# Kernel optimization log

Hardware: AMD Instinct MI355X
Metric: run time of the kernel (lower is better)

Reference implementation:

```python
import jax, jax.numpy as jnp
import numpy as np

N_USER, N_ITEM = 100000, 50000
D, H, B, E = 64, 64, 16384, 2000000

def _xavier(key, shape):
    fan_in, fan_out = shape[0], shape[1]
    lim = float(np.sqrt(6.0 / (fan_in + fan_out)))
    return jax.random.uniform(key, shape, jnp.float32, -lim, lim)

def setup_inputs() -> dict:
    key = jax.random.key(0)
    ks = jax.random.split(key, 16)
    inp = {
        "user_table": _xavier(ks[0], (N_USER, D)),
        "item_table": _xavier(ks[1], (N_ITEM, D)),
        "Wu": _xavier(ks[2], (D, D)),   # GCN_user weight ([in,out])
        "bu": jnp.zeros((D,), jnp.float32),
        "Wi": _xavier(ks[3], (D, D)),   # GCN_item weight
        "bi": jnp.zeros((D,), jnp.float32),
        "W1": _xavier(ks[4], (4 * D, 2 * H)),
        "b1": jnp.zeros((2 * H,), jnp.float32),
        "W2": _xavier(ks[5], (2 * H, H)),
        "b2": jnp.zeros((H,), jnp.float32),
        "W3": _xavier(ks[6], (H, 1)),
        "b3": jnp.zeros((1,), jnp.float32),
        "user_bias": jnp.zeros((N_USER, 1), jnp.float32),
        "item_bias": jnp.zeros((N_ITEM, 1), jnp.float32),
        "user_id": jax.random.randint(ks[7], (B,), 0, N_USER),
        "item_id": jax.random.randint(ks[8], (B,), 0, N_ITEM),
        "edge_user": jax.random.randint(ks[9], (E,), 0, N_USER),
        "edge_item": jax.random.randint(ks[10], (E,), 0, N_ITEM),
    }
    return inp

def reference(user_table, item_table, Wu, bu, Wi, bi, W1, b1, W2, b2, W3, b3,
              user_bias, item_bias, user_id, item_id, edge_user, edge_item):
    # sparse.mm(edge_ui, item_h)[user_id]: aggregate item embeddings per user
    agg_i = jax.ops.segment_sum(item_table[edge_item], edge_user, num_segments=N_USER)[user_id]
    agg_u = jax.ops.segment_sum(user_table[edge_user], edge_item, num_segments=N_ITEM)[item_id]
    ones_e = jnp.ones((edge_user.shape[0],), jnp.float32)
    deg_u = jax.ops.segment_sum(ones_e, edge_user, num_segments=N_USER)[user_id] + 1.0  # item_din
    deg_i = jax.ops.segment_sum(ones_e, edge_item, num_segments=N_ITEM)[item_id] + 1.0  # user_din
    gcn_item_h = agg_i / deg_u[:, None]   # [B, D]
    gcn_user_h = agg_u / deg_i[:, None]   # [B, D]
    # dropout p=0.3 is identity in eval mode
    gcn_user_out = jax.nn.relu(gcn_user_h @ Wu + bu)
    gcn_item_out = jax.nn.relu(gcn_item_h @ Wi + bi)
    u_emb = user_table[user_id]
    i_emb = item_table[item_id]
    x = jnp.concatenate([u_emb * i_emb,
                         u_emb * gcn_item_out,
                         gcn_user_out * i_emb,
                         gcn_user_out * gcn_item_out], axis=-1)  # [B, 4D]
    x1 = jnp.tanh(x @ W1 + b1)
    x2 = jnp.tanh(x1 @ W2 + b2)
    x3 = (x2 @ W3 + b3).reshape(-1)
    return x3 + user_bias[user_id, 0] + item_bias[item_id, 0]
```

## Files before the change

kernel.cpp:

```cpp
#include <hip/hip_runtime.h>
#include <cstdint>
#include <cstddef>

#define D 64
#define CAPU 96
#define CAPI 128
#define OCAP 4096
#define GR 32

__global__ __launch_bounds__(256) void k_build_maps(const int* __restrict__ user_id,
                                                    const int* __restrict__ item_id,
                                                    int* __restrict__ map_u,
                                                    int* __restrict__ map_i, int B)
{
    int i = blockIdx.x * blockDim.x + threadIdx.x;
    if (i < B) {
        atomicCAS(&map_u[user_id[i]], -1, i);
        atomicCAS(&map_i[item_id[i]], -1, i);
    }
}

__global__ __launch_bounds__(256) void k_scatter(const int* __restrict__ edge_user,
                                                 const int* __restrict__ edge_item,
                                                 const int* __restrict__ map_u,
                                                 const int* __restrict__ map_i,
                                                 int* __restrict__ cntU,
                                                 int* __restrict__ cntI,
                                                 uint32_t* __restrict__ listU,
                                                 uint32_t* __restrict__ listI,
                                                 int* __restrict__ ovfCnt,
                                                 uint32_t* __restrict__ ovf, int E)
{
    int t = blockIdx.x * blockDim.x + threadIdx.x;
    int base = t * 4;
    if (base >= E) return;

    int us[4], is[4];
    int cnt4 = 4;
    if (base + 3 < E) {
        int4 eu = *(const int4*)(edge_user + base);
        int4 ei = *(const int4*)(edge_item + base);
        us[0] = eu.x; us[1] = eu.y; us[2] = eu.z; us[3] = eu.w;
        is[0] = ei.x; is[1] = ei.y; is[2] = ei.z; is[3] = ei.w;
    } else {
        cnt4 = E - base;
        for (int q = 0; q < cnt4; ++q) { us[q] = edge_user[base + q]; is[q] = edge_item[base + q]; }
    }

    #pragma unroll
    for (int q = 0; q < 4; ++q) {
        if (q >= cnt4) break;
        int u = us[q], it = is[q];
        int su = map_u[u];
        int si = map_i[it];
        if (su >= 0) {
            int pos = atomicAdd(&cntU[su * 16], 1);
            if (pos < CAPU) listU[(size_t)su * CAPU + pos] = (uint32_t)it;
            else { int o = atomicAdd(ovfCnt, 1);
                   if (o < OCAP) ovf[o] = ((uint32_t)su << 17) | (uint32_t)it; }
        }
        if (si >= 0) {
            int pos = atomicAdd(&cntI[si * 16], 1);
            if (pos < CAPI) listI[(size_t)si * CAPI + pos] = (uint32_t)u;
            else { int o = atomicAdd(ovfCnt, 1);
                   if (o < OCAP) ovf[o] = 0x80000000u | ((uint32_t)si << 17) | (uint32_t)u; }
        }
    }
}

__global__ __launch_bounds__(256) void k_gather(const uint32_t* __restrict__ listU,
                                                const uint32_t* __restrict__ listI,
                                                const int* __restrict__ cntU,
                                                const int* __restrict__ cntI,
                                                const float* __restrict__ user_table,
                                                const float* __restrict__ item_table,
                                                const int* __restrict__ ovfCnt,
                                                const uint32_t* __restrict__ ovf,
                                                float* __restrict__ aggIU,
                                                float* __restrict__ aggUI, int B)
{
    int gg = (blockIdx.x * blockDim.x + threadIdx.x) >> 4;
    if (gg >= 2 * B) return;
    int l16 = threadIdx.x & 15;
    int side = gg >= B;
    int slot = side ? gg - B : gg;

    int cnt = side ? cntI[slot * 16] : cntU[slot * 16];
    int caps = side ? CAPI : CAPU;
    int n = cnt < caps ? cnt : caps;
    const uint32_t* list = side ? (listI + (size_t)slot * CAPI)
                                : (listU + (size_t)slot * CAPU);
    const float4* table4 = (const float4*)(side ? user_table : item_table);

    float4 a0 = {0.f, 0.f, 0.f, 0.f};
    float4 a1 = {0.f, 0.f, 0.f, 0.f};
    int j = 0;
    #pragma unroll 2
    for (; j + 2 <= n; j += 2) {
        int r0 = (int)list[j];
        int r1 = (int)list[j + 1];
        float4 v0 = table4[(size_t)r0 * 16 + l16];
        float4 v1 = table4[(size_t)r1 * 16 + l16];
        a0.x += v0.x; a0.y += v0.y; a0.z += v0.z; a0.w += v0.w;
        a1.x += v1.x; a1.y += v1.y; a1.z += v1.z; a1.w += v1.w;
    }
    if (j < n) {
        int r0 = (int)list[j];
        float4 v0 = table4[(size_t)r0 * 16 + l16];
        a0.x += v0.x; a0.y += v0.y; a0.z += v0.z; a0.w += v0.w;
    }
    if (cnt > caps) {
        int on = *ovfCnt; if (on > OCAP) on = OCAP;
        for (int k = 0; k < on; ++k) {
            uint32_t p = ovf[k];
            if ((int)(p >> 31) == side && (int)((p >> 17) & 0x3FFFu) == slot) {
                float4 v = table4[(size_t)(p & 0x1FFFFu) * 16 + l16];
                a0.x += v.x; a0.y += v.y; a0.z += v.z; a0.w += v.w;
            }
        }
    }
    float inv = 1.0f / ((float)cnt + 1.0f);
    float4 acc = {(a0.x + a1.x) * inv, (a0.y + a1.y) * inv,
                  (a0.z + a1.z) * inv, (a0.w + a1.w) * inv};
    float4* agg4 = (float4*)(side ? aggUI : aggIU);
    agg4[(size_t)slot * 16 + l16] = acc;
}

__global__ __launch_bounds__(256) void k_gcn(const int* __restrict__ user_id,
                                             const int* __restrict__ item_id,
                                             const int* __restrict__ map_u,
                                             const int* __restrict__ map_i,
                                             const float* __restrict__ aggIU,
                                             const float* __restrict__ aggUI,
                                             const float* __restrict__ Wi,
                                             const float* __restrict__ bi,
                                             const float* __restrict__ Wu,
                                             const float* __restrict__ bu,
                                             float* __restrict__ Xgi,
                                             float* __restrict__ Xgu, int B)
{
    __shared__ float A[GR][68];
    __shared__ float Wl[64][64];
    __shared__ int sslot[GR];
    int t = threadIdx.x;
    int nb = B / GR;
    int b = blockIdx.x;
    int side = b >= nb;
    int row0 = (side ? b - nb : b) * GR;

    if (t < GR) {
        int r = row0 + t;
        sslot[t] = side ? map_i[item_id[r]] : map_u[user_id[r]];
    }
    {
        const float4* Wg = (const float4*)(side ? Wu : Wi);
        float4* Wl4 = (float4*)&Wl[0][0];
        #pragma unroll
        for (int q = 0; q < 4; ++q) Wl4[t + q * 256] = Wg[t + q * 256];
    }
    __syncthreads();
    {
        const float4* agg4 = (const float4*)(side ? aggUI : aggIU);
        #pragma unroll
        for (int q = 0; q < 2; ++q) {
            int idx = t * 2 + q;
            int r = idx >> 4, l16 = idx & 15;
            ((float4*)&A[r][0])[l16] = agg4[(size_t)sslot[r] * 16 + l16];
        }
    }
    __syncthreads();

    const float* bias = side ? bu : bi;
    int tx = t & 15, ty = t >> 4;
    float acc[2][4] = {};
    for (int k = 0; k < 64; ++k) {
        float a0 = A[2 * ty][k];
        float a1 = A[2 * ty + 1][k];
        #pragma unroll
        for (int c = 0; c < 4; ++c) {
            float w = Wl[k][tx + 16 * c];
            acc[0][c] = fmaf(a0, w, acc[0][c]);
            acc[1][c] = fmaf(a1, w, acc[1][c]);
        }
    }
    float* Xg = side ? Xgu : Xgi;
    #pragma unroll
    for (int r = 0; r < 2; ++r) {
        int row = row0 + 2 * ty + r;
        #pragma unroll
        for (int c = 0; c < 4; ++c) {
            int col = tx + 16 * c;
            Xg[(size_t)row * 64 + col] = fmaxf(acc[r][c] + bias[col], 0.f);
        }
    }
}

__global__ __launch_bounds__(256) void k_mlp(const int* __restrict__ user_id,
                                             const int* __restrict__ item_id,
                                             const float* __restrict__ user_table,
                                             const float* __restrict__ item_table,
                                             const float* __restrict__ Xgi,
                                             const float* __restrict__ Xgu,
                                             const float* __restrict__ W1,
                                             const float* __restrict__ b1,
                                             const float* __restrict__ W2,
                                             const float* __restrict__ b2,
                                             const float* __restrict__ W3,
                                             const float* __restrict__ b3,
                                             const float* __restrict__ user_bias,
                                             const float* __restrict__ item_bias,
                                             float* __restrict__ out, int B)
{
    __shared__ float Fbuf[64][68];
    __shared__ float WB[8192];
    __shared__ int sU[GR], sI[GR];
    int t = threadIdx.x;
    int row0 = blockIdx.x * GR;
    if (t < GR) { sU[t] = user_id[row0 + t]; sI[t] = item_id[row0 + t]; }
    __syncthreads();

    int tx1 = t & 31, ty1 = t >> 5;
    float acc1[4][4] = {};

    const int fkA[4] = {0, 0, 3, 3};
    const int fkB[4] = {1, 2, 1, 2};
    for (int j = 0; j < 4; ++j) {
        #pragma unroll
        for (int half = 0; half < 2; ++half) {
            int kind = half ? fkB[j] : fkA[j];
            #pragma unroll
            for (int q = 0; q < 2; ++q) {
                int idx = t * 2 + q;
                int r = idx >> 4, l16 = idx & 15;
                const float4* src;
                size_t rowidx;
                if (kind == 0)      { src = (const float4*)user_table; rowidx = (size_t)sU[r]; }
                else if (kind == 1) { src = (const float4*)item_table; rowidx = (size_t)sI[r]; }
                else if (kind == 2) { src = (const float4*)Xgi; rowidx = (size_t)(row0 + r); }
                else                { src = (const float4*)Xgu; rowidx = (size_t)(row0 + r); }
                ((float4*)&Fbuf[half * 32 + r][0])[l16] = src[rowidx * 16 + l16];
            }
        }
        {
            const float4* w4 = (const float4*)W1 + (size_t)j * 2048;
            float4* d = (float4*)WB;
            #pragma unroll
            for (int q = 0; q < 8; ++q) d[t + q * 256] = w4[t + q * 256];
        }
        __syncthreads();
        for (int k = 0; k < 64; ++k) {
            float a[4], b[4];
            #pragma unroll
            for (int r = 0; r < 4; ++r)
                a[r] = Fbuf[4 * ty1 + r][k] * Fbuf[32 + 4 * ty1 + r][k];
            #pragma unroll
            for (int c = 0; c < 4; ++c) b[c] = WB[k * 128 + tx1 + 32 * c];
            #pragma unroll
            for (int r = 0; r < 4; ++r)
                #pragma unroll
                for (int c = 0; c < 4; ++c)
                    acc1[r][c] = fmaf(a[r], b[c], acc1[r][c]);
        }
        __syncthreads();
    }

    float* x1t = &Fbuf[0][0];
    #pragma unroll
    for (int r = 0; r < 4; ++r)
        #pragma unroll
        for (int c = 0; c < 4; ++c) {
            int col = tx1 + 32 * c;
            x1t[(4 * ty1 + r) * 132 + col] = tanhf(acc1[r][c] + b1[col]);
        }
    {
        const float4* w4 = (const float4*)W2;
        float4* d = (float4*)WB;
        #pragma unroll
        for (int q = 0; q < 8; ++q) d[t + q * 256] = w4[t + q * 256];
    }
    __syncthreads();

    int tx2 = t & 15, ty2 = t >> 4;
    float acc2[2][4] = {};
    for (int k = 0; k < 128; ++k) {
        float a0 = x1t[(2 * ty2) * 132 + k];
        float a1 = x1t[(2 * ty2 + 1) * 132 + k];
        #pragma unroll
        for (int c = 0; c < 4; ++c) {
            float w = WB[k * 64 + tx2 + 16 * c];
            acc2[0][c] = fmaf(a0, w, acc2[0][c]);
            acc2[1][c] = fmaf(a1, w, acc2[1][c]);
        }
    }
    float b3v = b3[0];
    #pragma unroll
    for (int r = 0; r < 2; ++r) {
        int lr = 2 * ty2 + r;
        float p = 0.f;
        #pragma unroll
        for (int c = 0; c < 4; ++c) {
            int col = tx2 + 16 * c;
            p += tanhf(acc2[r][c] + b2[col]) * W3[col];
        }
        p += __shfl_xor(p, 1);
        p += __shfl_xor(p, 2);
        p += __shfl_xor(p, 4);
        p += __shfl_xor(p, 8);
        if (tx2 == 0)
            out[row0 + lr] = p + b3v + user_bias[sU[lr]] + item_bias[sI[lr]];
    }
}

extern "C" void kernel_launch(void* const* d_in, const int* in_sizes, int n_in,
                              void* d_out, int out_size, void* d_ws, size_t ws_size,
                              hipStream_t stream)
{
    const float* user_table = (const float*)d_in[0];
    const float* item_table = (const float*)d_in[1];
    const float* Wu = (const float*)d_in[2];
    const float* bu = (const float*)d_in[3];
    const float* Wi = (const float*)d_in[4];
    const float* bi = (const float*)d_in[5];
    const float* W1 = (const float*)d_in[6];
    const float* b1 = (const float*)d_in[7];
    const float* W2 = (const float*)d_in[8];
    const float* b2 = (const float*)d_in[9];
    const float* W3 = (const float*)d_in[10];
    const float* b3 = (const float*)d_in[11];
    const float* user_bias = (const float*)d_in[12];
    const float* item_bias = (const float*)d_in[13];
    const int* user_id = (const int*)d_in[14];
    const int* item_id = (const int*)d_in[15];
    const int* edge_user = (const int*)d_in[16];
    const int* edge_item = (const int*)d_in[17];

    const int N_USER = in_sizes[0] / D;
    const int N_ITEM = in_sizes[1] / D;
    const int B = in_sizes[14];
    const int E = in_sizes[16];

    char* ws = (char*)d_ws;
    size_t off = 0;
    const size_t aggIU_off = off; off += (size_t)B * D * 4;
    const size_t aggUI_off = off; off += (size_t)B * D * 4;
    const size_t mapu_off  = off; off += (size_t)N_USER * 4;
    const size_t mapi_off  = off; off += (size_t)N_ITEM * 4;
    const size_t cntU_off  = off; off += (size_t)B * 16 * 4;
    const size_t cntI_off  = off; off += (size_t)B * 16 * 4;
    const size_t ovfc_off  = off; off += 256;
    const size_t ovf_off   = off; off += (size_t)OCAP * 4;
    const size_t listU_off = off; off += (size_t)B * CAPU * 4;
    const size_t listI_off = off; off += (size_t)B * CAPI * 4;

    float* aggIU = (float*)(ws + aggIU_off);
    float* aggUI = (float*)(ws + aggUI_off);
    int*   map_u = (int*)(ws + mapu_off);
    int*   map_i = (int*)(ws + mapi_off);
    int*   cntU  = (int*)(ws + cntU_off);
    int*   cntI  = (int*)(ws + cntI_off);
    int*   ovfCnt = (int*)(ws + ovfc_off);
    uint32_t* ovf = (uint32_t*)(ws + ovf_off);
    uint32_t* listU = (uint32_t*)(ws + listU_off);
    uint32_t* listI = (uint32_t*)(ws + listI_off);
    float* Xgi = (float*)(ws + listU_off);
    float* Xgu = Xgi + (size_t)B * D;

    hipMemsetAsync(ws + mapu_off, 0xFF, (size_t)(N_USER + N_ITEM) * 4, stream);
    hipMemsetAsync(ws + cntU_off, 0, (size_t)B * 16 * 4 * 2 + 256 + OCAP * 4, stream);

    k_build_maps<<<(B + 255) / 256, 256, 0, stream>>>(user_id, item_id, map_u, map_i, B);

    k_scatter<<<(E / 4 + 255) / 256, 256, 0, stream>>>(edge_user, edge_item, map_u, map_i,
                                                       cntU, cntI, listU, listI, ovfCnt, ovf, E);

    k_gather<<<(2 * B) / 16, 256, 0, stream>>>(listU, listI, cntU, cntI,
                                               user_table, item_table, ovfCnt, ovf,
                                               aggIU, aggUI, B);

    k_gcn<<<2 * (B / GR), 256, 0, stream>>>(user_id, item_id, map_u, map_i,
                                            aggIU, aggUI, Wi, bi, Wu, bu, Xgi, Xgu, B);

    k_mlp<<<B / GR, 256, 0, stream>>>(user_id, item_id, user_table, item_table,
                                      Xgi, Xgu, W1, b1, W2, b2, W3, b3,
                                      user_bias, item_bias, (float*)d_out, B);
}
```

Measured before the change: 242.7 us.

## Fuse GCN projection into MLP kernel and widen scatter/gather per-thread work

Merges the GCN linear+ReLU kernel into the MLP kernel, keeping the GCN outputs in shared memory instead of writing them to global memory and reading them back. This saves one launch and the global round trip, but raises shared memory use per block, which may lower occupancy. The scatter kernel now handles 8 edges per thread and loads all map lookups before issuing the atomics. The gather kernel unrolls to 4 independent accumulators to get more loads in flight.

Result: slower. 250.4 us (+3.2%).

```diff
diff --git a/kernel.cpp b/kernel.cpp
--- a/kernel.cpp
+++ b/kernel.cpp
@@ -32,38 +32,46 @@
                                                  uint32_t* __restrict__ ovf, int E)
 {
     int t = blockIdx.x * blockDim.x + threadIdx.x;
-    int base = t * 4;
+    int base = t * 8;
     if (base >= E) return;
 
-    int us[4], is[4];
-    int cnt4 = 4;
-    if (base + 3 < E) {
-        int4 eu = *(const int4*)(edge_user + base);
-        int4 ei = *(const int4*)(edge_item + base);
-        us[0] = eu.x; us[1] = eu.y; us[2] = eu.z; us[3] = eu.w;
-        is[0] = ei.x; is[1] = ei.y; is[2] = ei.z; is[3] = ei.w;
+    int us[8], is[8];
+    int cnt8 = 8;
+    if (base + 8 <= E) {
+        int4 eu0 = *(const int4*)(edge_user + base);
+        int4 eu1 = *(const int4*)(edge_user + base + 4);
+        int4 ei0 = *(const int4*)(edge_item + base);
+        int4 ei1 = *(const int4*)(edge_item + base + 4);
+        us[0]=eu0.x; us[1]=eu0.y; us[2]=eu0.z; us[3]=eu0.w;
+        us[4]=eu1.x; us[5]=eu1.y; us[6]=eu1.z; us[7]=eu1.w;
+        is[0]=ei0.x; is[1]=ei0.y; is[2]=ei0.z; is[3]=ei0.w;
+        is[4]=ei1.x; is[5]=ei1.y; is[6]=ei1.z; is[7]=ei1.w;
     } else {
-        cnt4 = E - base;
-        for (int q = 0; q < cnt4; ++q) { us[q] = edge_user[base + q]; is[q] = edge_item[base + q]; }
-    }
-
-    #pragma unroll
-    for (int q = 0; q < 4; ++q) {
-        if (q >= cnt4) break;
-        int u = us[q], it = is[q];
-        int su = map_u[u];
-        int si = map_i[it];
-        if (su >= 0) {
-            int pos = atomicAdd(&cntU[su * 16], 1);
-            if (pos < CAPU) listU[(size_t)su * CAPU + pos] = (uint32_t)it;
+        cnt8 = E - base;
+        for (int q = 0; q < cnt8; ++q) { us[q] = edge_user[base + q]; is[q] = edge_item[base + q]; }
+    }
+
+    int su[8], si[8];
+    #pragma unroll
+    for (int q = 0; q < 8; ++q) {
+        if (q >= cnt8) break;
+        su[q] = map_u[us[q]];
+        si[q] = map_i[is[q]];
+    }
+    #pragma unroll
+    for (int q = 0; q < 8; ++q) {
+        if (q >= cnt8) break;
+        if (su[q] >= 0) {
+            int pos = atomicAdd(&cntU[su[q] * 16], 1);
+            if (pos < CAPU) listU[(size_t)su[q] * CAPU + pos] = (uint32_t)is[q];
             else { int o = atomicAdd(ovfCnt, 1);
-                   if (o < OCAP) ovf[o] = ((uint32_t)su << 17) | (uint32_t)it; }
-        }
-        if (si >= 0) {
-            int pos = atomicAdd(&cntI[si * 16], 1);
-            if (pos < CAPI) listI[(size_t)si * CAPI + pos] = (uint32_t)u;
+                   if (o < OCAP) ovf[o] = ((uint32_t)su[q] << 17) | (uint32_t)is[q]; }
+        }
+        if (si[q] >= 0) {
+            int pos = atomicAdd(&cntI[si[q] * 16], 1);
+            if (pos < CAPI) listI[(size_t)si[q] * CAPI + pos] = (uint32_t)us[q];
             else { int o = atomicAdd(ovfCnt, 1);
-                   if (o < OCAP) ovf[o] = 0x80000000u | ((uint32_t)si << 17) | (uint32_t)u; }
+                   if (o < OCAP) ovf[o] = 0x80000000u | ((uint32_t)si[q] << 17) | (uint32_t)us[q]; }
         }
     }
 }
@@ -92,19 +100,21 @@
                                 : (listU + (size_t)slot * CAPU);
     const float4* table4 = (const float4*)(side ? user_table : item_table);
 
-    float4 a0 = {0.f, 0.f, 0.f, 0.f};
-    float4 a1 = {0.f, 0.f, 0.f, 0.f};
+    float4 a0 = {0.f,0.f,0.f,0.f}, a1 = {0.f,0.f,0.f,0.f};
+    float4 a2 = {0.f,0.f,0.f,0.f}, a3 = {0.f,0.f,0.f,0.f};
     int j = 0;
-    #pragma unroll 2
-    for (; j + 2 <= n; j += 2) {
-        int r0 = (int)list[j];
-        int r1 = (int)list[j + 1];
+    for (; j + 4 <= n; j += 4) {
+        int r0 = (int)list[j], r1 = (int)list[j+1], r2 = (int)list[j+2], r3 = (int)list[j+3];
         float4 v0 = table4[(size_t)r0 * 16 + l16];
         float4 v1 = table4[(size_t)r1 * 16 + l16];
+        float4 v2 = table4[(size_t)r2 * 16 + l16];
+        float4 v3 = table4[(size_t)r3 * 16 + l16];
         a0.x += v0.x; a0.y += v0.y; a0.z += v0.z; a0.w += v0.w;
         a1.x += v1.x; a1.y += v1.y; a1.z += v1.z; a1.w += v1.w;
-    }
-    if (j < n) {
+        a2.x += v2.x; a2.y += v2.y; a2.z += v2.z; a2.w += v2.w;
+        a3.x += v3.x; a3.y += v3.y; a3.z += v3.z; a3.w += v3.w;
+    }
+    for (; j < n; ++j) {
         int r0 = (int)list[j];
         float4 v0 = table4[(size_t)r0 * 16 + l16];
         a0.x += v0.x; a0.y += v0.y; a0.z += v0.z; a0.w += v0.w;
@@ -120,98 +130,37 @@
         }
     }
     float inv = 1.0f / ((float)cnt + 1.0f);
-    float4 acc = {(a0.x + a1.x) * inv, (a0.y + a1.y) * inv,
-                  (a0.z + a1.z) * inv, (a0.w + a1.w) * inv};
+    float4 acc = {(a0.x+a1.x+a2.x+a3.x) * inv, (a0.y+a1.y+a2.y+a3.y) * inv,
+                  (a0.z+a1.z+a2.z+a3.z) * inv, (a0.w+a1.w+a2.w+a3.w) * inv};
     float4* agg4 = (float4*)(side ? aggUI : aggIU);
     agg4[(size_t)slot * 16 + l16] = acc;
 }
 
-__global__ __launch_bounds__(256) void k_gcn(const int* __restrict__ user_id,
-                                             const int* __restrict__ item_id,
-                                             const int* __restrict__ map_u,
-                                             const int* __restrict__ map_i,
-                                             const float* __restrict__ aggIU,
-                                             const float* __restrict__ aggUI,
-                                             const float* __restrict__ Wi,
-                                             const float* __restrict__ bi,
-                                             const float* __restrict__ Wu,
-                                             const float* __restrict__ bu,
-                                             float* __restrict__ Xgi,
-                                             float* __restrict__ Xgu, int B)
-{
-    __shared__ float A[GR][68];
-    __shared__ float Wl[64][64];
-    __shared__ int sslot[GR];
-    int t = threadIdx.x;
-    int nb = B / GR;
-    int b = blockIdx.x;
-    int side = b >= nb;
-    int row0 = (side ? b - nb : b) * GR;
-
-    if (t < GR) {
-        int r = row0 + t;
-        sslot[t] = side ? map_i[item_id[r]] : map_u[user_id[r]];
-    }
-    {
-        const float4* Wg = (const float4*)(side ? Wu : Wi);
-        float4* Wl4 = (float4*)&Wl[0][0];
-        #pragma unroll
-        for (int q = 0; q < 4; ++q) Wl4[t + q * 256] = Wg[t + q * 256];
-    }
-    __syncthreads();
-    {
-        const float4* agg4 = (const float4*)(side ? aggUI : aggIU);
-        #pragma unroll
-        for (int q = 0; q < 2; ++q) {
-            int idx = t * 2 + q;
-            int r = idx >> 4, l16 = idx & 15;
-            ((float4*)&A[r][0])[l16] = agg4[(size_t)sslot[r] * 16 + l16];
-        }
-    }
-    __syncthreads();
-
-    const float* bias = side ? bu : bi;
-    int tx = t & 15, ty = t >> 4;
-    float acc[2][4] = {};
-    for (int k = 0; k < 64; ++k) {
-        float a0 = A[2 * ty][k];
-        float a1 = A[2 * ty + 1][k];
-        #pragma unroll
-        for (int c = 0; c < 4; ++c) {
-            float w = Wl[k][tx + 16 * c];
-            acc[0][c] = fmaf(a0, w, acc[0][c]);
-            acc[1][c] = fmaf(a1, w, acc[1][c]);
-        }
-    }
-    float* Xg = side ? Xgu : Xgi;
-    #pragma unroll
-    for (int r = 0; r < 2; ++r) {
-        int row = row0 + 2 * ty + r;
-        #pragma unroll
-        for (int c = 0; c < 4; ++c) {
-            int col = tx + 16 * c;
-            Xg[(size_t)row * 64 + col] = fmaxf(acc[r][c] + bias[col], 0.f);
-        }
-    }
-}
-
-__global__ __launch_bounds__(256) void k_mlp(const int* __restrict__ user_id,
-                                             const int* __restrict__ item_id,
-                                             const float* __restrict__ user_table,
-                                             const float* __restrict__ item_table,
-                                             const float* __restrict__ Xgi,
-                                             const float* __restrict__ Xgu,
-                                             const float* __restrict__ W1,
-                                             const float* __restrict__ b1,
-                                             const float* __restrict__ W2,
-                                             const float* __restrict__ b2,
-                                             const float* __restrict__ W3,
-                                             const float* __restrict__ b3,
-                                             const float* __restrict__ user_bias,
-                                             const float* __restrict__ item_bias,
-                                             float* __restrict__ out, int B)
-{
-    __shared__ float Fbuf[64][68];
+__global__ __launch_bounds__(256) void k_gcn_mlp(const int* __restrict__ user_id,
+                                                 const int* __restrict__ item_id,
+                                                 const int* __restrict__ map_u,
+                                                 const int* __restrict__ map_i,
+                                                 const float* __restrict__ aggIU,
+                                                 const float* __restrict__ aggUI,
+                                                 const float* __restrict__ user_table,
+                                                 const float* __restrict__ item_table,
+                                                 const float* __restrict__ Wi,
+                                                 const float* __restrict__ bi,
+                                                 const float* __restrict__ Wu,
+                                                 const float* __restrict__ bu,
+                                                 const float* __restrict__ W1,
+                                                 const float* __restrict__ b1,
+                                                 const float* __restrict__ W2,
+                                                 const float* __restrict__ b2,
+                                                 const float* __restrict__ W3,
+                                                 const float* __restrict__ b3,
+                                                 const float* __restrict__ user_bias,
+                                                 const float* __restrict__ item_bias,
+                                                 float* __restrict__ out, int B)
+{
+    __shared__ float XgiL[GR][68];
+    __shared__ float XguL[GR][68];
+    __shared__ float Fbuf[2 * GR][68];
     __shared__ float WB[8192];
     __shared__ int sU[GR], sI[GR];
     int t = threadIdx.x;
@@ -219,28 +168,82 @@
     if (t < GR) { sU[t] = user_id[row0 + t]; sI[t] = item_id[row0 + t]; }
     __syncthreads();
 
+    int txg = t & 15, tyg = t >> 4;
+    {
+        const float4* agg4 = (const float4*)aggIU;
+        #pragma unroll
+        for (int q = 0; q < 2; ++q) {
+            int idx = t * 2 + q; int r = idx >> 4, l16 = idx & 15;
+            int slot = map_u[sU[r]];
+            ((float4*)&Fbuf[r][0])[l16] = agg4[(size_t)slot * 16 + l16];
+        }
+        const float4* wg = (const float4*)Wi;
+        float4* d = (float4*)WB;
+        #pragma unroll
+        for (int q = 0; q < 4; ++q) d[t + q * 256] = wg[t + q * 256];
+    }
+    __syncthreads();
+    {
+        float acc[2][4] = {};
+        for (int k = 0; k < 64; ++k) {
+            float a0 = Fbuf[2 * tyg][k], a1 = Fbuf[2 * tyg + 1][k];
+            #pragma unroll
+            for (int c = 0; c < 4; ++c) {
+                float w = WB[k * 64 + txg + 16 * c];
+                acc[0][c] = fmaf(a0, w, acc[0][c]);
+                acc[1][c] = fmaf(a1, w, acc[1][c]);
+            }
+        }
+        #pragma unroll
+        for (int r = 0; r < 2; ++r)
+            #pragma unroll
+            for (int c = 0; c < 4; ++c)
+                XgiL[2 * tyg + r][txg + 16 * c] = fmaxf(acc[r][c] + bi[txg + 16 * c], 0.f);
+    }
+    __syncthreads();
+    {
+        const float4* agg4 = (const float4*)aggUI;
+        #pragma unroll
+        for (int q = 0; q < 2; ++q) {
+            int idx = t * 2 + q; int r = idx >> 4, l16 = idx & 15;
+            int slot = map_i[sI[r]];
+            ((float4*)&Fbuf[r][0])[l16] = agg4[(size_t)slot * 16 + l16];
+        }
+        const float4* wg = (const float4*)Wu;
+        float4* d = (float4*)WB;
+        #pragma unroll
+        for (int q = 0; q < 4; ++q) d[t + q * 256] = wg[t + q * 256];
+    }
+    __syncthreads();
+    {
+        float acc[2][4] = {};
+        for (int k = 0; k < 64; ++k) {
+            float a0 = Fbuf[2 * tyg][k], a1 = Fbuf[2 * tyg + 1][k];
+            #pragma unroll
+            for (int c = 0; c < 4; ++c) {
+                float w = WB[k * 64 + txg + 16 * c];
+                acc[0][c] = fmaf(a0, w, acc[0][c]);
+                acc[1][c] = fmaf(a1, w, acc[1][c]);
+            }
+        }
+        #pragma unroll
+        for (int r = 0; r < 2; ++r)
+            #pragma unroll
+            for (int c = 0; c < 4; ++c)
+                XguL[2 * tyg + r][txg + 16 * c] = fmaxf(acc[r][c] + bu[txg + 16 * c], 0.f);
+    }
+    __syncthreads();
+
+    #pragma unroll
+    for (int q = 0; q < 2; ++q) {
+        int idx = t * 2 + q; int r = idx >> 4, l16 = idx & 15;
+        ((float4*)&Fbuf[r][0])[l16] = ((const float4*)user_table)[(size_t)sU[r] * 16 + l16];
+        ((float4*)&Fbuf[GR + r][0])[l16] = ((const float4*)item_table)[(size_t)sI[r] * 16 + l16];
+    }
+
     int tx1 = t & 31, ty1 = t >> 5;
     float acc1[4][4] = {};
-
-    const int fkA[4] = {0, 0, 3, 3};
-    const int fkB[4] = {1, 2, 1, 2};
     for (int j = 0; j < 4; ++j) {
-        #pragma unroll
-        for (int half = 0; half < 2; ++half) {
-            int kind = half ? fkB[j] : fkA[j];
-            #pragma unroll
-            for (int q = 0; q < 2; ++q) {
-                int idx = t * 2 + q;
-                int r = idx >> 4, l16 = idx & 15;
-                const float4* src;
-                size_t rowidx;
-                if (kind == 0)      { src = (const float4*)user_table; rowidx = (size_t)sU[r]; }
-                else if (kind == 1) { src = (const float4*)item_table; rowidx = (size_t)sI[r]; }
-                else if (kind == 2) { src = (const float4*)Xgi; rowidx = (size_t)(row0 + r); }
-                else                { src = (const float4*)Xgu; rowidx = (size_t)(row0 + r); }
-                ((float4*)&Fbuf[half * 32 + r][0])[l16] = src[rowidx * 16 + l16];
-            }
-        }
         {
             const float4* w4 = (const float4*)W1 + (size_t)j * 2048;
             float4* d = (float4*)WB;
@@ -248,11 +251,12 @@
             for (int q = 0; q < 8; ++q) d[t + q * 256] = w4[t + q * 256];
         }
         __syncthreads();
+        const float (*FA)[68] = (j < 2) ? (const float (*)[68])&Fbuf[0] : (const float (*)[68])XguL;
+        const float (*FB)[68] = ((j & 1) == 0) ? (const float (*)[68])&Fbuf[GR] : (const float (*)[68])XgiL;
         for (int k = 0; k < 64; ++k) {
             float a[4], b[4];
             #pragma unroll
-            for (int r = 0; r < 4; ++r)
-                a[r] = Fbuf[4 * ty1 + r][k] * Fbuf[32 + 4 * ty1 + r][k];
+            for (int r = 0; r < 4; ++r) a[r] = FA[4 * ty1 + r][k] * FB[4 * ty1 + r][k];
             #pragma unroll
             for (int c = 0; c < 4; ++c) b[c] = WB[k * 128 + tx1 + 32 * c];
             #pragma unroll
@@ -362,25 +366,21 @@
     uint32_t* ovf = (uint32_t*)(ws + ovf_off);
     uint32_t* listU = (uint32_t*)(ws + listU_off);
     uint32_t* listI = (uint32_t*)(ws + listI_off);
-    float* Xgi = (float*)(ws + listU_off);
-    float* Xgu = Xgi + (size_t)B * D;
 
     hipMemsetAsync(ws + mapu_off, 0xFF, (size_t)(N_USER + N_ITEM) * 4, stream);
     hipMemsetAsync(ws + cntU_off, 0, (size_t)B * 16 * 4 * 2 + 256 + OCAP * 4, stream);
 
     k_build_maps<<<(B + 255) / 256, 256, 0, stream>>>(user_id, item_id, map_u, map_i, B);
 
-    k_scatter<<<(E / 4 + 255) / 256, 256, 0, stream>>>(edge_user, edge_item, map_u, map_i,
+    k_scatter<<<(E / 8 + 255) / 256, 256, 0, stream>>>(edge_user, edge_item, map_u, map_i,
                                                        cntU, cntI, listU, listI, ovfCnt, ovf, E);
 
     k_gather<<<(2 * B) / 16, 256, 0, stream>>>(listU, listI, cntU, cntI,
                                                user_table, item_table, ovfCnt, ovf,
                                                aggIU, aggUI, B);
 
-    k_gcn<<<2 * (B / GR), 256, 0, stream>>>(user_id, item_id, map_u, map_i,
-                                            aggIU, aggUI, Wi, bi, Wu, bu, Xgi, Xgu, B);
-
-    k_mlp<<<B / GR, 256, 0, stream>>>(user_id, item_id, user_table, item_table,
-                                      Xgi, Xgu, W1, b1, W2, b2, W3, b3,
-                                      user_bias, item_bias, (float*)d_out, B);
-}
+    k_gcn_mlp<<<B / GR, 256, 0, stream>>>(user_id, item_id, map_u, map_i,
+                                          aggIU, aggUI, user_table, item_table,
+                                          Wi, bi, Wu, bu, W1, b1, W2, b2, W3, b3,
+                                          user_bias, item_bias, (float*)d_out, B);
+}
```
